# Kernel tuning notes

Measured on AMD Instinct MI355X. Metric: run time of the kernel, lower is better.

The kernel has to match this reference:

```python
import jax, jax.numpy as jnp
import numpy as np


def silu(x):
    return x * jax.nn.sigmoid(x)


def setup_inputs() -> dict:
    key = jax.random.key(0)
    B, L, Din = 2, 512, 128
    E, K = 2, 4
    d = E * Din          # inner dim = 256
    N = d                # state size forced to hid_dim = expansion*input_dim
    R = d // 16          # dt low-rank = 16
    ks = jax.random.split(key, 12)
    s = 0.02
    rn = lambda k, sh: (jax.random.normal(k, sh, jnp.float32) * s)
    return {
        "x":      jax.random.normal(ks[0], (B, L, Din), jnp.float32),
        "W_in":   rn(ks[1], (Din, d)),  "b_in":  jnp.zeros((d,), jnp.float32),
        "W_res":  rn(ks[2], (Din, d)),  "b_res": jnp.zeros((d,), jnp.float32),
        "conv_w": rn(ks[3], (d, d, K)), "conv_b": jnp.zeros((d,), jnp.float32),
        "W_xdt":  rn(ks[4], (d, R)),
        "W_dt":   rn(ks[5], (R, d)),
        "b_dt":   jnp.full((d,), -4.6, jnp.float32),  # softplus -> dt ~ 0.01
        "W_B":    rn(ks[6], (d, N)),
        "W_C":    rn(ks[7], (d, N)),
        "A_log":  jnp.log(jnp.broadcast_to(jnp.arange(1, N + 1, dtype=jnp.float32), (d, N))),
        "D":      jnp.ones((d,), jnp.float32),
        "W_out":  rn(ks[8], (d, Din)), "b_out": jnp.zeros((Din,), jnp.float32),
    }


def reference(x, W_in, b_in, W_res, b_res, conv_w, conv_b,
              W_xdt, W_dt, b_dt, W_B, W_C, A_log, D, W_out, b_out):
    k = conv_w.shape[-1]
    # input projections
    xi = x @ W_in + b_in               # [B,L,d]
    x_res = silu(x @ W_res + b_res)    # [B,L,d] gate branch
    # causal full (groups=1) conv1d: padding k-1, truncated to length L
    c = jax.lax.conv_general_dilated(
        xi.transpose(0, 2, 1), conv_w, window_strides=(1,),
        padding=[(k - 1, 0)], dimension_numbers=("NCH", "OIH", "NCH"))
    u = silu((c + conv_b[None, :, None]).transpose(0, 2, 1))  # [B,L,d]
    # S6 selective scan
    delta = jax.nn.softplus((u @ W_xdt) @ W_dt + b_dt)  # [B,L,d]
    Bm = u @ W_B                                        # [B,L,N]
    Cm = u @ W_C                                        # [B,L,N]
    A = -jnp.exp(A_log)                                 # [d,N]

    def step(h, xs):
        u_t, d_t, B_t, C_t = xs                         # [B,d],[B,d],[B,N],[B,N]
        dA = jnp.exp(d_t[:, :, None] * A)               # [B,d,N]
        h = dA * h + (d_t * u_t)[:, :, None] * B_t[:, None, :]
        y = jnp.einsum("bdn,bn->bd", h, C_t)
        return h, y

    h0 = jnp.zeros((x.shape[0], A.shape[0], A.shape[1]), xi.dtype)
    xs = (u.transpose(1, 0, 2), delta.transpose(1, 0, 2),
          Bm.transpose(1, 0, 2), Cm.transpose(1, 0, 2))
    _, ys = jax.lax.scan(step, h0, xs)                  # ys: [L,B,d]
    y = ys.transpose(1, 0, 2) + u * D                   # skip connection D*u
    # residual gate + output projection (norm disabled)
    return (y + x_res) @ W_out + b_out
```

## Files before the change

kernel.cpp:

```cpp
#include <hip/hip_runtime.h>
#include <hip/hip_bf16.h>

#define kB   2
#define kL   512
#define kBL  1024
#define kDin 128
#define kD   256
#define kN   256
#define kR   16
#define kK   4
#define kS   8
#define kT   64

__device__ __forceinline__ float silu_f(float v) { return v / (1.f + __expf(-v)); }
__device__ __forceinline__ float softplus_f(float z) {
    return (z > 20.f) ? z : log1pf(__expf(z));
}
__device__ __forceinline__ float4 f4fma(float s, float4 w, float4 a) {
    a.x += s * w.x; a.y += s * w.y; a.z += s * w.z; a.w += s * w.w; return a;
}

__global__ void __launch_bounds__(256) pre_kernel(
        const float* __restrict__ x, const float* __restrict__ W_in,
        const float* __restrict__ b_in, const float* __restrict__ W_res,
        const float* __restrict__ b_res, const float* __restrict__ conv_w,
        float* __restrict__ wT, float* __restrict__ xi, float* __restrict__ xres) {
    __shared__ float tile[32][33];
    __shared__ float xs[2][kDin];
    __shared__ float red[128][9];
    int bid = blockIdx.x, tid = threadIdx.x;
    if (bid < 256) {
        int c0 = (bid & 31) * 32, r0 = (bid >> 5) * 32;
        int tx = tid & 31, ty = tid >> 5;
        #pragma unroll
        for (int j = 0; j < 32; j += 8)
            tile[ty + j][tx] = conv_w[(r0 + ty + j) * 1024 + c0 + tx];
        __syncthreads();
        #pragma unroll
        for (int j = 0; j < 32; j += 8)
            wT[(c0 + ty + j) * 256 + r0 + tx] = tile[tx][ty + j];
        return;
    }
    int bt0 = (bid - 256) * 2;
    xs[tid >> 7][tid & 127] = x[bt0 * kDin + tid];
    __syncthreads();
    int q = tid & 63, m = (tid >> 6) & 1, ks = tid >> 7;
    const float* W = m ? W_res : W_in;
    float4 a0 = {0,0,0,0}, a1 = {0,0,0,0};
    int i0 = ks * 64;
    #pragma unroll 4
    for (int i = i0; i < i0 + 64; i++) {
        float4 w = ((const float4*)(W + i * kD))[q];
        a0 = f4fma(xs[0][i], w, a0);
        a1 = f4fma(xs[1][i], w, a1);
    }
    if (ks) {
        float* rr = red[tid - 128];
        rr[0] = a0.x; rr[1] = a0.y; rr[2] = a0.z; rr[3] = a0.w;
        rr[4] = a1.x; rr[5] = a1.y; rr[6] = a1.z; rr[7] = a1.w;
    }
    __syncthreads();
    if (!ks) {
        const float* rr = red[tid];
        a0.x += rr[0]; a0.y += rr[1]; a0.z += rr[2]; a0.w += rr[3];
        a1.x += rr[4]; a1.y += rr[5]; a1.z += rr[6]; a1.w += rr[7];
        float4 bv = ((const float4*)(m ? b_res : b_in))[q];
        a0.x += bv.x; a0.y += bv.y; a0.z += bv.z; a0.w += bv.w;
        a1.x += bv.x; a1.y += bv.y; a1.z += bv.z; a1.w += bv.w;
        if (m) {
            float4 s0 = {silu_f(a0.x), silu_f(a0.y), silu_f(a0.z), silu_f(a0.w)};
            float4 s1 = {silu_f(a1.x), silu_f(a1.y), silu_f(a1.z), silu_f(a1.w)};
            ((float4*)(xres + (bt0 + 0) * kD))[q] = s0;
            ((float4*)(xres + (bt0 + 1) * kD))[q] = s1;
        } else {
            ((float4*)(xi + (bt0 + 0) * kD))[q] = a0;
            ((float4*)(xi + (bt0 + 1) * kD))[q] = a1;
        }
    }
}

__global__ void __launch_bounds__(512) conv_fwd(
        const float* __restrict__ xi, const float* __restrict__ wT,
        const float* __restrict__ conv_b, float* __restrict__ u) {
    __shared__ float xs[7][kD];
    __shared__ float red[7][64][17];
    int bid = blockIdx.x, tid = threadIdx.x;
    int b = bid >> 7, t0 = (bid & 127) * 4;
    for (int idx = tid; idx < 7 * kD; idx += 512) {
        int j = idx >> 8, i = idx & 255;
        int t = t0 - 3 + j;
        xs[j][i] = (t >= 0) ? xi[(b * kL + t) * kD + i] : 0.f;
    }
    __syncthreads();
    int q = tid & 63, ks = tid >> 6;
    float4 a[4] = {{0,0,0,0},{0,0,0,0},{0,0,0,0},{0,0,0,0}};
    int ik0 = ks * 128;
    #pragma unroll 4
    for (int ik = ik0; ik < ik0 + 128; ik++) {
        float4 w = ((const float4*)(wT + ik * kD))[q];
        int ii = ik >> 2, k = ik & 3;
        #pragma unroll
        for (int r = 0; r < 4; r++) a[r] = f4fma(xs[k + r][ii], w, a[r]);
    }
    if (ks) {
        float* rr = red[ks - 1][q];
        #pragma unroll
        for (int r = 0; r < 4; r++) {
            rr[4*r+0] = a[r].x; rr[4*r+1] = a[r].y;
            rr[4*r+2] = a[r].z; rr[4*r+3] = a[r].w;
        }
    }
    __syncthreads();
    if (!ks) {
        #pragma unroll
        for (int p = 0; p < 7; p++) {
            const float* rr = red[p][q];
            #pragma unroll
            for (int r = 0; r < 4; r++) {
                a[r].x += rr[4*r+0]; a[r].y += rr[4*r+1];
                a[r].z += rr[4*r+2]; a[r].w += rr[4*r+3];
            }
        }
        float4 cb = ((const float4*)conv_b)[q];
        #pragma unroll
        for (int r = 0; r < 4; r++) {
            float4 v = {silu_f(a[r].x + cb.x), silu_f(a[r].y + cb.y),
                        silu_f(a[r].z + cb.z), silu_f(a[r].w + cb.w)};
            ((float4*)(u + (b * kL + t0 + r) * kD))[q] = v;
        }
    }
}

__global__ void __launch_bounds__(256) proj_bcd(
        const float* __restrict__ u, const float* __restrict__ W_xdt,
        const float* __restrict__ W_dt, const float* __restrict__ b_dt,
        const float* __restrict__ W_B, const float* __restrict__ W_C,
        float* __restrict__ delta, float* __restrict__ Bm, float* __restrict__ Cm) {
    __shared__ float us[2][kD];
    __shared__ float tpart[128];
    __shared__ float ts[2][kR];
    __shared__ float red[128][9];
    int bt0 = blockIdx.x * 2, tid = threadIdx.x;
    us[0][tid] = u[(bt0 + 0) * kD + tid];
    us[1][tid] = u[(bt0 + 1) * kD + tid];
    __syncthreads();
    if (tid < 128) {
        int r = tid >> 6, j = (tid >> 2) & 15, kq = tid & 3;
        float acc = 0.f;
        #pragma unroll 4
        for (int i = kq * 64; i < kq * 64 + 64; i++)
            acc += us[r][i] * W_xdt[i * kR + j];
        tpart[tid] = acc;
    }
    __syncthreads();
    if (tid < 32) {
        int r = tid >> 4, j = tid & 15;
        int base = r * 64 + j * 4;
        ts[r][j] = tpart[base] + tpart[base+1] + tpart[base+2] + tpart[base+3];
    }
    __syncthreads();
    int q = tid & 63, m = (tid >> 6) & 1, ks = tid >> 7;
    const float* W = m ? W_C : W_B;
    float4 a0 = {0,0,0,0}, a1 = {0,0,0,0};
    int i0 = ks * 128;
    #pragma unroll 4
    for (int i = i0; i < i0 + 128; i++) {
        float4 w = ((const float4*)(W + i * kN))[q];
        a0 = f4fma(us[0][i], w, a0);
        a1 = f4fma(us[1][i], w, a1);
    }
    if (ks) {
        float* rr = red[tid - 128];
        rr[0] = a0.x; rr[1] = a0.y; rr[2] = a0.z; rr[3] = a0.w;
        rr[4] = a1.x; rr[5] = a1.y; rr[6] = a1.z; rr[7] = a1.w;
    }
    __syncthreads();
    if (!ks) {
        const float* rr = red[tid];
        a0.x += rr[0]; a0.y += rr[1]; a0.z += rr[2]; a0.w += rr[3];
        a1.x += rr[4]; a1.y += rr[5]; a1.z += rr[6]; a1.w += rr[7];
        float* O = m ? Cm : Bm;
        ((float4*)(O + (bt0 + 0) * kN))[q] = a0;
        ((float4*)(O + (bt0 + 1) * kN))[q] = a1;
    }
    if (tid < 64) {
        float4 d0 = {0,0,0,0}, d1 = {0,0,0,0};
        #pragma unroll
        for (int j = 0; j < kR; j++) {
            float4 w = ((const float4*)(W_dt + j * kD))[tid];
            d0 = f4fma(ts[0][j], w, d0);
            d1 = f4fma(ts[1][j], w, d1);
        }
        float4 bd = ((const float4*)b_dt)[tid];
        float4 o0 = {softplus_f(d0.x + bd.x), softplus_f(d0.y + bd.y),
                     softplus_f(d0.z + bd.z), softplus_f(d0.w + bd.w)};
        float4 o1 = {softplus_f(d1.x + bd.x), softplus_f(d1.y + bd.y),
                     softplus_f(d1.z + bd.z), softplus_f(d1.w + bd.w)};
        ((float4*)(delta + (bt0 + 0) * kD))[tid] = o0;
        ((float4*)(delta + (bt0 + 1) * kD))[tid] = o1;
    }
}

__global__ void __launch_bounds__(512) scan_fused(
        const float* __restrict__ delta, const float* __restrict__ u,
        const float* __restrict__ Bm, const float* __restrict__ Cm,
        const float* __restrict__ A_log, float* __restrict__ ys) {
    __shared__ float hpart[kS][kN];
    __shared__ float dsumS[kS];
    int d = blockIdx.x & 255;
    int b = blockIdx.x >> 8;
    int s    = threadIdx.x >> 6;
    int lane = threadIdx.x & 63;

    float4 al = ((const float4*)(A_log + d * kN))[lane];
    float A0 = -__expf(al.x), A1 = -__expf(al.y);
    float A2 = -__expf(al.z), A3 = -__expf(al.w);

    int gtu = (b * kL + s * kT + lane) * kD + d;
    float my_dt = delta[gtu];
    float my_u  = u[gtu];
    float my_du = my_dt * my_u;

    float dsum = my_dt;
    #pragma unroll
    for (int off = 32; off; off >>= 1) dsum += __shfl_xor(dsum, off, 64);

    const float4* Bp = (const float4*)(Bm + (b * kL + s * kT) * kN) + lane;
    const float4* Cp = (const float4*)(Cm + (b * kL + s * kT) * kN) + lane;

    float h0 = 0, h1 = 0, h2 = 0, h3 = 0;
    for (int t = 0; t < kT; t++) {
        float dt = __shfl(my_dt, t, 64);
        float du = __shfl(my_du, t, 64);
        float4 B4 = Bp[t * (kN / 4)];
        h0 = __expf(dt * A0) * h0 + du * B4.x;
        h1 = __expf(dt * A1) * h1 + du * B4.y;
        h2 = __expf(dt * A2) * h2 + du * B4.z;
        h3 = __expf(dt * A3) * h3 + du * B4.w;
    }
    hpart[s][4 * lane + 0] = h0;
    hpart[s][4 * lane + 1] = h1;
    hpart[s][4 * lane + 2] = h2;
    hpart[s][4 * lane + 3] = h3;
    if (lane == 0) dsumS[s] = dsum;
    __syncthreads();

    h0 = h1 = h2 = h3 = 0;
    float P = 0.f;
    for (int j = s - 1; j >= 0; j--) {
        h0 += __expf(A0 * P) * hpart[j][4 * lane + 0];
        h1 += __expf(A1 * P) * hpart[j][4 * lane + 1];
        h2 += __expf(A2 * P) * hpart[j][4 * lane + 2];
        h3 += __expf(A3 * P) * hpart[j][4 * lane + 3];
        P += dsumS[j];
    }

    float* yp = ys + (b * kL + s * kT) * kD + d;
    for (int t = 0; t < kT; t++) {
        float dt = __shfl(my_dt, t, 64);
        float du = __shfl(my_du, t, 64);
        float4 B4 = Bp[t * (kN / 4)];
        float4 C4 = Cp[t * (kN / 4)];
        h0 = __expf(dt * A0) * h0 + du * B4.x;
        h1 = __expf(dt * A1) * h1 + du * B4.y;
        h2 = __expf(dt * A2) * h2 + du * B4.z;
        h3 = __expf(dt * A3) * h3 + du * B4.w;
        float y = h0 * C4.x + h1 * C4.y + h2 * C4.z + h3 * C4.w;
        #pragma unroll
        for (int off = 32; off; off >>= 1) y += __shfl_xor(y, off, 64);
        if (lane == 0) yp[t * kD] = y;
    }
}

__global__ void __launch_bounds__(256) out_proj(
        const float* __restrict__ ys, const float* __restrict__ u,
        const float* __restrict__ Dv, const float* __restrict__ xres,
        const float* __restrict__ W_out, const float* __restrict__ b_out,
        float* __restrict__ out) {
    __shared__ float vs[2][kD];
    __shared__ float red[224][9];
    int bt0 = blockIdx.x * 2, tid = threadIdx.x;
    for (int idx = tid; idx < 512; idx += 256) {
        int r = idx >> 8, i = idx & 255;
        int g = (bt0 + r) * kD + i;
        vs[r][i] = ys[g] + u[g] * Dv[i] + xres[g];
    }
    __syncthreads();
    int q = tid & 31, ks = tid >> 5;
    float4 a0 = {0,0,0,0}, a1 = {0,0,0,0};
    int i0 = ks * 32;
    #pragma unroll 4
    for (int i = i0; i < i0 + 32; i++) {
        float4 w = ((const float4*)(W_out + i * kDin))[q];
        a0 = f4fma(vs[0][i], w, a0);
        a1 = f4fma(vs[1][i], w, a1);
    }
    if (ks) {
        float* rr = red[tid - 32];
        rr[0] = a0.x; rr[1] = a0.y; rr[2] = a0.z; rr[3] = a0.w;
        rr[4] = a1.x; rr[5] = a1.y; rr[6] = a1.z; rr[7] = a1.w;
    }
    __syncthreads();
    if (!ks) {
        #pragma unroll
        for (int p = 0; p < 7; p++) {
            const float* rr = red[p * 32 + tid];
            a0.x += rr[0]; a0.y += rr[1]; a0.z += rr[2]; a0.w += rr[3];
            a1.x += rr[4]; a1.y += rr[5]; a1.z += rr[6]; a1.w += rr[7];
        }
        float4 bv = ((const float4*)b_out)[q];
        a0.x += bv.x; a0.y += bv.y; a0.z += bv.z; a0.w += bv.w;
        a1.x += bv.x; a1.y += bv.y; a1.z += bv.z; a1.w += bv.w;
        ((float4*)(out + (bt0 + 0) * kDin))[q] = a0;
        ((float4*)(out + (bt0 + 1) * kDin))[q] = a1;
    }
}

extern "C" void kernel_launch(void* const* d_in, const int* in_sizes, int n_in,
                              void* d_out, int out_size, void* d_ws, size_t ws_size,
                              hipStream_t stream) {
    const float* x      = (const float*)d_in[0];
    const float* W_in   = (const float*)d_in[1];
    const float* b_in   = (const float*)d_in[2];
    const float* W_res  = (const float*)d_in[3];
    const float* b_res  = (const float*)d_in[4];
    const float* conv_w = (const float*)d_in[5];
    const float* conv_b = (const float*)d_in[6];
    const float* W_xdt  = (const float*)d_in[7];
    const float* W_dt   = (const float*)d_in[8];
    const float* b_dt   = (const float*)d_in[9];
    const float* W_B    = (const float*)d_in[10];
    const float* W_C    = (const float*)d_in[11];
    const float* A_log  = (const float*)d_in[12];
    const float* Dv     = (const float*)d_in[13];
    const float* W_out  = (const float*)d_in[14];
    const float* b_out  = (const float*)d_in[15];

    float* ws    = (float*)d_ws;
    float* slot0 = ws;
    float* xres  = ws + 1 * 262144;
    float* slot2 = ws + 2 * 262144;
    float* u     = ws + 3 * 262144;
    float* yss   = ws + 4 * 262144;
    float* Cmat  = ws + 5 * 262144;

    float* xi    = slot0;
    float* delta = slot0;
    float* wT    = slot2;
    float* Bmat  = slot2;

    pre_kernel<<<768, 256, 0, stream>>>(x, W_in, b_in, W_res, b_res, conv_w,
                                        wT, xi, xres);
    conv_fwd<<<256, 512, 0, stream>>>(xi, wT, conv_b, u);
    proj_bcd<<<512, 256, 0, stream>>>(u, W_xdt, W_dt, b_dt, W_B, W_C,
                                      delta, Bmat, Cmat);
    scan_fused<<<kB * kD, 512, 0, stream>>>(delta, u, Bmat, Cmat, A_log, yss);
    out_proj<<<512, 256, 0, stream>>>(yss, u, Dv, xres, W_out, b_out,
                                      (float*)d_out);
}
```

Measured before the change: 181.7 us.

## Process two channels per scan block and batch timesteps by four

The scan kernel now handles two d channels per 1024-thread block and stages dt and du in shared memory instead of broadcasting them with per-step shuffles. Each timestep loop is processed in chunks of four, so the B/C loads and exps are issued ahead of the recurrence, which exposes more independent work. Output y values are collected per lane and written in one coalesced-per-lane store instead of lane-0 strided writes. Blocks are larger and fewer (256 instead of 512), which may lower occupancy and increases register pressure from the unrolled arrays.

```diff
diff --git a/kernel.cpp b/kernel.cpp
--- a/kernel.cpp
+++ b/kernel.cpp
@@ -201,16 +201,18 @@
     }
 }
 
-__global__ void __launch_bounds__(512) scan_fused(
+__global__ void __launch_bounds__(1024) scan_fused(
         const float* __restrict__ delta, const float* __restrict__ u,
         const float* __restrict__ Bm, const float* __restrict__ Cm,
         const float* __restrict__ A_log, float* __restrict__ ys) {
-    __shared__ float hpart[kS][kN];
-    __shared__ float dsumS[kS];
-    int d = blockIdx.x & 255;
-    int b = blockIdx.x >> 8;
-    int s    = threadIdx.x >> 6;
-    int lane = threadIdx.x & 63;
+    __shared__ float4 hp4[2][kS][64];
+    __shared__ float dt_s[16][kT];
+    __shared__ float du_s[16][kT];
+    __shared__ float dsumS[2][kS];
+    int w = threadIdx.x >> 6, lane = threadIdx.x & 63;
+    int s = w & 7, dd = w >> 3;
+    int b = blockIdx.x >> 7, dp = blockIdx.x & 127;
+    int d = dp * 2 + dd;
 
     float4 al = ((const float4*)(A_log + d * kN))[lane];
     float A0 = -__expf(al.x), A1 = -__expf(al.y);
@@ -218,58 +220,92 @@
 
     int gtu = (b * kL + s * kT + lane) * kD + d;
     float my_dt = delta[gtu];
-    float my_u  = u[gtu];
-    float my_du = my_dt * my_u;
+    float my_du = my_dt * u[gtu];
 
     float dsum = my_dt;
     #pragma unroll
     for (int off = 32; off; off >>= 1) dsum += __shfl_xor(dsum, off, 64);
 
+    dt_s[w][lane] = my_dt;
+    du_s[w][lane] = my_du;
+
     const float4* Bp = (const float4*)(Bm + (b * kL + s * kT) * kN) + lane;
     const float4* Cp = (const float4*)(Cm + (b * kL + s * kT) * kN) + lane;
+    __syncthreads();
 
     float h0 = 0, h1 = 0, h2 = 0, h3 = 0;
-    for (int t = 0; t < kT; t++) {
-        float dt = __shfl(my_dt, t, 64);
-        float du = __shfl(my_du, t, 64);
-        float4 B4 = Bp[t * (kN / 4)];
-        h0 = __expf(dt * A0) * h0 + du * B4.x;
-        h1 = __expf(dt * A1) * h1 + du * B4.y;
-        h2 = __expf(dt * A2) * h2 + du * B4.z;
-        h3 = __expf(dt * A3) * h3 + du * B4.w;
-    }
-    hpart[s][4 * lane + 0] = h0;
-    hpart[s][4 * lane + 1] = h1;
-    hpart[s][4 * lane + 2] = h2;
-    hpart[s][4 * lane + 3] = h3;
-    if (lane == 0) dsumS[s] = dsum;
+    for (int c = 0; c < kT; c += 4) {
+        float4 dt4 = *(const float4*)&dt_s[w][c];
+        float4 du4 = *(const float4*)&du_s[w][c];
+        float4 Bb[4];
+        #pragma unroll
+        for (int j = 0; j < 4; j++) Bb[j] = Bp[(c + j) * (kN / 4)];
+        float dts[4] = {dt4.x, dt4.y, dt4.z, dt4.w};
+        float dus[4] = {du4.x, du4.y, du4.z, du4.w};
+        float e[4][4];
+        #pragma unroll
+        for (int j = 0; j < 4; j++) {
+            e[j][0] = __expf(dts[j] * A0);
+            e[j][1] = __expf(dts[j] * A1);
+            e[j][2] = __expf(dts[j] * A2);
+            e[j][3] = __expf(dts[j] * A3);
+        }
+        #pragma unroll
+        for (int j = 0; j < 4; j++) {
+            h0 = e[j][0] * h0 + dus[j] * Bb[j].x;
+            h1 = e[j][1] * h1 + dus[j] * Bb[j].y;
+            h2 = e[j][2] * h2 + dus[j] * Bb[j].z;
+            h3 = e[j][3] * h3 + dus[j] * Bb[j].w;
+        }
+    }
+    hp4[dd][s][lane] = make_float4(h0, h1, h2, h3);
+    if (lane == 0) dsumS[dd][s] = dsum;
     __syncthreads();
 
     h0 = h1 = h2 = h3 = 0;
     float P = 0.f;
     for (int j = s - 1; j >= 0; j--) {
-        h0 += __expf(A0 * P) * hpart[j][4 * lane + 0];
-        h1 += __expf(A1 * P) * hpart[j][4 * lane + 1];
-        h2 += __expf(A2 * P) * hpart[j][4 * lane + 2];
-        h3 += __expf(A3 * P) * hpart[j][4 * lane + 3];
-        P += dsumS[j];
-    }
-
-    float* yp = ys + (b * kL + s * kT) * kD + d;
-    for (int t = 0; t < kT; t++) {
-        float dt = __shfl(my_dt, t, 64);
-        float du = __shfl(my_du, t, 64);
-        float4 B4 = Bp[t * (kN / 4)];
-        float4 C4 = Cp[t * (kN / 4)];
-        h0 = __expf(dt * A0) * h0 + du * B4.x;
-        h1 = __expf(dt * A1) * h1 + du * B4.y;
-        h2 = __expf(dt * A2) * h2 + du * B4.z;
-        h3 = __expf(dt * A3) * h3 + du * B4.w;
-        float y = h0 * C4.x + h1 * C4.y + h2 * C4.z + h3 * C4.w;
-        #pragma unroll
-        for (int off = 32; off; off >>= 1) y += __shfl_xor(y, off, 64);
-        if (lane == 0) yp[t * kD] = y;
-    }
+        float4 hv = hp4[dd][j][lane];
+        h0 += __expf(A0 * P) * hv.x;
+        h1 += __expf(A1 * P) * hv.y;
+        h2 += __expf(A2 * P) * hv.z;
+        h3 += __expf(A3 * P) * hv.w;
+        P += dsumS[dd][j];
+    }
+
+    float my_y = 0.f;
+    for (int c = 0; c < kT; c += 4) {
+        float4 dt4 = *(const float4*)&dt_s[w][c];
+        float4 du4 = *(const float4*)&du_s[w][c];
+        float4 Bb[4], Cc[4];
+        #pragma unroll
+        for (int j = 0; j < 4; j++) {
+            Bb[j] = Bp[(c + j) * (kN / 4)];
+            Cc[j] = Cp[(c + j) * (kN / 4)];
+        }
+        float dts[4] = {dt4.x, dt4.y, dt4.z, dt4.w};
+        float dus[4] = {du4.x, du4.y, du4.z, du4.w};
+        float e[4][4];
+        #pragma unroll
+        for (int j = 0; j < 4; j++) {
+            e[j][0] = __expf(dts[j] * A0);
+            e[j][1] = __expf(dts[j] * A1);
+            e[j][2] = __expf(dts[j] * A2);
+            e[j][3] = __expf(dts[j] * A3);
+        }
+        #pragma unroll
+        for (int j = 0; j < 4; j++) {
+            h0 = e[j][0] * h0 + dus[j] * Bb[j].x;
+            h1 = e[j][1] * h1 + dus[j] * Bb[j].y;
+            h2 = e[j][2] * h2 + dus[j] * Bb[j].z;
+            h3 = e[j][3] * h3 + dus[j] * Bb[j].w;
+            float y = h0 * Cc[j].x + h1 * Cc[j].y + h2 * Cc[j].z + h3 * Cc[j].w;
+            #pragma unroll
+            for (int off = 32; off; off >>= 1) y += __shfl_xor(y, off, 64);
+            my_y = (lane == c + j) ? y : my_y;
+        }
+    }
+    ys[(b * kL + s * kT + lane) * kD + d] = my_y;
 }
 
 __global__ void __launch_bounds__(256) out_proj(
@@ -354,7 +390,7 @@
     conv_fwd<<<256, 512, 0, stream>>>(xi, wT, conv_b, u);
     proj_bcd<<<512, 256, 0, stream>>>(u, W_xdt, W_dt, b_dt, W_B, W_C,
                                       delta, Bmat, Cmat);
-    scan_fused<<<kB * kD, 512, 0, stream>>>(delta, u, Bmat, Cmat, A_log, yss);
+    scan_fused<<<kB * 128, 1024, 0, stream>>>(delta, u, Bmat, Cmat, A_log, yss);
     out_proj<<<512, 256, 0, stream>>>(yss, u, Dv, xres, W_out, b_out,
                                       (float*)d_out);
 }
```

After: 171.6 us. -5.5%, faster.
